# Performance work log

Hardware: AMD Instinct MI355X
Metric: run time of the kernel (lower is better)

Reference implementation:

```python
import jax, jax.numpy as jnp
from jax import lax
import numpy as np

OUTS = [5, 1, 2, 2, 1, 1, 1, 1]  # heatmap, conf, dxy, wh, dist, offset, severity, surface
OFFS = np.concatenate([[0], np.cumsum(OUTS)])
BN_EPS = 1e-5


def setup_inputs() -> dict:
    key = jax.random.key(0)
    ks = jax.random.split(key, 10)
    N, C, Hf, Wf = 16, 576, 12, 20
    f = jax.random.normal(ks[0], (N, C, Hf, Wf), jnp.float32)
    det_w1 = jax.random.normal(ks[1], (8, C, C, 3, 3), jnp.float32) * 0.02
    det_bn_g = 1.0 + 0.1 * jax.random.normal(ks[2], (8, C), jnp.float32)
    det_bn_b = 0.1 * jax.random.normal(ks[3], (8, C), jnp.float32)
    det_bn_m = 0.1 * jax.random.normal(ks[4], (8, C), jnp.float32)
    det_bn_v = jax.random.uniform(ks[5], (8, C), jnp.float32) + 0.5
    det_w2 = jax.random.normal(ks[6], (14, C), jnp.float32) * 0.05
    det_b2 = jax.random.normal(ks[7], (14,), jnp.float32) * 0.05
    lin_W = jax.random.normal(ks[8], (10, C), jnp.float32) * 0.05
    lin_b = jnp.zeros((10,), jnp.float32)
    return dict(f=f, det_w1=det_w1, det_bn_g=det_bn_g, det_bn_b=det_bn_b,
                det_bn_m=det_bn_m, det_bn_v=det_bn_v, det_w2=det_w2, det_b2=det_b2,
                lin_W=lin_W, lin_b=lin_b, frame_w=640, frame_h=384)


def _head(f, w1, g, b, m, v, w2, b2):
    # conv3x3 (no bias) -> BN (inference) -> SiLU -> conv1x1
    dn = ('NCHW', 'OIHW', 'NCHW')
    h = lax.conv_general_dilated(f, w1, (1, 1), 'SAME', dimension_numbers=dn)
    scale = g * lax.rsqrt(v + BN_EPS)
    h = h * scale[None, :, None, None] + (b - m * scale)[None, :, None, None]
    h = h * jax.nn.sigmoid(h)  # SiLU
    return jnp.einsum('nchw,oc->nohw', h, w2) + b2[None, :, None, None]


def _forward(f, det_w1, det_bn_g, det_bn_b, det_bn_m, det_bn_v, det_w2, det_b2,
             lin_W, lin_b, frame_w, frame_h, max_dets=20):
    N, C, Hf, Wf = f.shape
    eps = 1e-5
    # ---- legacy single-hazard head from pooled features ----
    f1 = f.mean(axis=(2, 3))                      # [N, 576]  (AdaptiveAvgPool2d(1))
    lin = f1 @ lin_W.T + lin_b                    # [N, 10]
    conf = jnp.clip(jax.nn.sigmoid(lin[:, 0:1]), eps, 1.0 - eps)
    type_log = lin[:, 1:6]
    dist_m = jax.nn.sigmoid(lin[:, 6:7]) * 3.0
    offset = jnp.tanh(lin[:, 7:8])
    severity = jnp.clip(jax.nn.sigmoid(lin[:, 8:9]), eps, 1.0 - eps)
    surface = jnp.clip(jax.nn.sigmoid(lin[:, 9:10]), eps, 1.0 - eps)
    type_id = jnp.argmax(type_log, axis=1, keepdims=True).astype(f.dtype)
    single_out = jnp.concatenate([conf, type_id, dist_m, offset, severity, surface], axis=1)

    # ---- dense per-pixel heads ----
    maps = []
    for i in range(8):
        o0, o1 = int(OFFS[i]), int(OFFS[i + 1])
        maps.append(_head(f, det_w1[i], det_bn_g[i], det_bn_b[i],
                          det_bn_m[i], det_bn_v[i], det_w2[o0:o1], det_b2[o0:o1]))
    heat = jax.nn.sigmoid(maps[0])                # [N,5,H,W]
    conf_d = jax.nn.sigmoid(maps[1])              # [N,1,H,W]
    dxy = jax.nn.sigmoid(maps[2])                 # [N,2,H,W]
    wh = jax.nn.sigmoid(maps[3])                  # [N,2,H,W]
    dist = jax.nn.sigmoid(maps[4]) * 3.0          # [N,1,H,W]
    offsm = jnp.tanh(maps[5])
    sev = jax.nn.sigmoid(maps[6])
    surf = jax.nn.sigmoid(maps[7])

    # ---- per-class topk decode ----
    score_flat = (conf_d * heat).reshape(N, 5, Hf * Wf)
    k = min(max_dets, Hf * Wf)
    topk_scores, topk_idx = lax.top_k(score_flat, k)          # [N,5,k]
    top_scores = topk_scores.reshape(N, -1)                    # [N,5k]
    top_class = jnp.broadcast_to(jnp.arange(5, dtype=f.dtype)[None, :, None], (N, 5, k)).reshape(N, -1)
    idx_flat = topk_idx.reshape(N, -1)                          # [N,5k]
    y_idx = (idx_flat // Wf).astype(f.dtype)
    x_idx = (idx_flat % Wf).astype(f.dtype)

    g1 = lambda m: jnp.take_along_axis(m.reshape(N, -1), idx_flat, axis=1)
    gx, gy = g1(dxy[:, 0]), g1(dxy[:, 1])
    gw, gh = g1(wh[:, 0]), g1(wh[:, 1])
    gdist, goffs = g1(dist), g1(offsm)
    gsev, gsurf = g1(sev), g1(surf)

    stride_x = frame_w / Wf
    stride_y = frame_h / Hf
    cx = jnp.clip(x_idx + gx, 0, Wf - 1) * stride_x
    cy = jnp.clip(y_idx + gy, 0, Hf - 1) * stride_y
    bw = jnp.clip(gw, 0, 1) * frame_w
    bh = jnp.clip(gh, 0, 1) * frame_h
    x1 = jnp.clip(cx - bw / 2, 0, frame_w - 1)
    y1 = jnp.clip(cy - bh / 2, 0, frame_h - 1)
    x2 = jnp.clip(cx + bw / 2, 0, frame_w - 1)
    y2 = jnp.clip(cy + bh / 2, 0, frame_h - 1)

    dets = jnp.stack([top_scores, top_class, gdist, goffs, gsev, gsurf, x1, y1, x2, y2], axis=-1)  # [N,5k,10]
    order = jnp.argsort(dets[:, :, 2], axis=-1)   # ascending distance (nearest first)
    dets_sorted = jnp.take_along_axis(dets, order[:, :, None], axis=1)
    dets_out = dets_sorted[:, :max_dets, :]        # [N,K,10]
    return single_out, dets_out


def reference(f, det_w1, det_bn_g, det_bn_b, det_bn_m, det_bn_v, det_w2, det_b2,
              lin_W, lin_b, frame_w, frame_h):
    return _forward(f, det_w1, det_bn_g, det_bn_b, det_bn_m, det_bn_v,
                    det_w2, det_b2, lin_W, lin_b, frame_w, frame_h)
```

## Files before the change

### kernel.cpp

```cpp
#include <hip/hip_runtime.h>
#include <math.h>

#define NB 16
#define CC 576
#define HH 12
#define WW 20
#define PP 240
#define MM 3840
#define NHEAD 8
#define HALO 22

typedef __attribute__((ext_vector_type(8))) short short8;
typedef __attribute__((ext_vector_type(4))) float floatx4;
typedef unsigned short ushort_t;

__device__ __forceinline__ float sigmoidf_(float x) {
    return 1.0f / (1.0f + expf(-x));
}
__device__ __forceinline__ unsigned short f2bf(float x) {
    union { float f; unsigned u; } v; v.f = x;
    unsigned r = v.u + 0x7fff + ((v.u >> 16) & 1);
    return (unsigned short)(r >> 16);
}
__device__ __forceinline__ float bf2f(unsigned short b) {
    union { float f; unsigned u; } v; v.u = ((unsigned)b) << 16;
    return v.f;
}

__global__ __launch_bounds__(256) void k_single(const float* __restrict__ f1sum,
                                                const float* __restrict__ linW,
                                                const float* __restrict__ linb,
                                                float* __restrict__ out) {
    int n = blockIdx.x;
    __shared__ float lin[10];
    int t = threadIdx.x;
    int lane = t & 63, wave = t >> 6;
    const float inv = 1.0f / PP;
    for (int o = wave; o < 10; o += 4) {
        const float* wrow = linW + o * CC;
        float s = 0.f;
        for (int c = lane; c < CC; c += 64)
            s = fmaf(f1sum[n * CC + c] * inv, wrow[c], s);
        #pragma unroll
        for (int off = 32; off; off >>= 1) s += __shfl_xor(s, off, 64);
        if (lane == 0) lin[o] = s + linb[o];
    }
    __syncthreads();
    if (t == 0) {
        const float eps = 1e-5f;
        float conf = sigmoidf_(lin[0]);
        conf = fminf(fmaxf(conf, eps), 1.f - eps);
        int best = 0; float bv = lin[1];
        #pragma unroll
        for (int j = 1; j < 5; ++j) { if (lin[1 + j] > bv) { bv = lin[1 + j]; best = j; } }
        float dist = 3.f * sigmoidf_(lin[6]);
        float offs = tanhf(lin[7]);
        float sev  = fminf(fmaxf(sigmoidf_(lin[8]), eps), 1.f - eps);
        float surf = fminf(fmaxf(sigmoidf_(lin[9]), eps), 1.f - eps);
        float* o = out + n * 6;
        o[0] = conf; o[1] = (float)best; o[2] = dist;
        o[3] = offs; o[4] = sev; o[5] = surf;
    }
}

__global__ __launch_bounds__(256) void k_prep_f(const float* __restrict__ f,
                                                ushort_t* __restrict__ fhi,
                                                ushort_t* __restrict__ flo,
                                                float* __restrict__ f1sum) {
    __shared__ float tile[32][33];
    int c0 = blockIdx.x * 32, p0 = blockIdx.y * 32, n = blockIdx.z;
    int tp = threadIdx.x & 31, tc8 = threadIdx.x >> 5;
    for (int cc = tc8; cc < 32; cc += 8) {
        int p = p0 + tp;
        tile[cc][tp] = (p < PP) ? f[((size_t)n * CC + c0 + cc) * PP + p] : 0.f;
    }
    __syncthreads();
    if (threadIdx.x < 32) {
        float s = 0.f;
        #pragma unroll
        for (int pp = 0; pp < 32; ++pp) s += tile[threadIdx.x][pp];
        atomicAdd(&f1sum[n * CC + c0 + threadIdx.x], s);
    }
    int tcw = threadIdx.x & 31, tpw = threadIdx.x >> 5;
    for (int pp = tpw; pp < 32; pp += 8) {
        int p = p0 + pp;
        if (p < PP) {
            float v = tile[tcw][pp];
            unsigned short hi = f2bf(v);
            size_t o = ((size_t)n * PP + p) * CC + c0 + tcw;
            fhi[o] = hi;
            flo[o] = f2bf(v - bf2f(hi));
        }
    }
}

__global__ __launch_bounds__(256) void k_prep_w(const float* __restrict__ w1,
                                                ushort_t* __restrict__ whi,
                                                ushort_t* __restrict__ wlo) {
    __shared__ float ws[288 * 33];
    int b = blockIdx.x;
    int cib = b % 18;
    int rest = b / 18;
    int half = rest & 1;
    int hc = rest >> 1;
    int t = threadIdx.x;
    const float* src = w1
        + ((size_t)(hc / 9) * CC + (hc % 9) * 64 + half * 32) * (CC * 9)
        + (size_t)cib * 288;
    for (int i = t; i < 32 * 288; i += 256) {
        int co = i / 288, k = i - co * 288;
        ws[k * 33 + co] = src[(size_t)co * (CC * 9) + k];
    }
    __syncthreads();
    size_t obase = ((size_t)hc * 18 + cib) * 18432 + (size_t)half * 1024;
    for (int idx = t; idx < 9 * 2 * 64; idx += 256) {
        int tap = idx / 128, r = idx - tap * 128;
        int jj = r >> 6, lane = r & 63;
        int col = jj * 16 + (lane & 15);
        int krow = (lane >> 4) * 8;
        short8 vh, vl;
        #pragma unroll
        for (int e = 0; e < 8; ++e) {
            float v = ws[((krow + e) * 9 + tap) * 33 + col];
            unsigned short hi = f2bf(v);
            vh[e] = (short)hi;
            vl[e] = (short)f2bf(v - bf2f(hi));
        }
        size_t o = obase + (size_t)tap * 2048 + jj * 512 + lane * 8;
        *(short8*)(whi + o) = vh;
        *(short8*)(wlo + o) = vl;
    }
}

__global__ __launch_bounds__(256, 3) void k_conv_mfma(
        const ushort_t* __restrict__ fhi, const ushort_t* __restrict__ flo,
        const ushort_t* __restrict__ whi, const ushort_t* __restrict__ wlo,
        const float* __restrict__ w2,
        const float* __restrict__ bng, const float* __restrict__ bnb,
        const float* __restrict__ bnm, const float* __restrict__ bnv,
        float* __restrict__ maps) {
    __shared__ __align__(16) ushort_t Ah[1216 * 8];
    __shared__ __align__(16) ushort_t Al[1216 * 8];
    __shared__ ushort_t rowmap[9 * 256];

    int t = threadIdx.x;

    int bid = blockIdx.x;
    int xcd = bid & 7;
    int q = bid >> 3;
    int mt = q % 15;
    int slice = (q / 15) * 8 + xcd;
    int m0 = mt * 256;
    int c0b = slice % 9;
    int c0 = c0b * 64;
    int h  = slice / 9;

    int w = t >> 6, lane = t & 63;
    int quad = lane >> 4, l15 = lane & 15;
    int srow_lo = t & 15, sg = (t >> 4) & 3, srb = t >> 6;

    const ushort_t* bp_h = whi + (size_t)(h * 9 + c0b) * 331776 + lane * 8;
    const ushort_t* bp_l = wlo + (size_t)(h * 9 + c0b) * 331776 + lane * 8;

    short8 cbh[4], cbl[4];
    #pragma unroll
    for (int j = 0; j < 4; ++j) {
        cbh[j] = *(const short8*)(bp_h + j * 512);
        cbl[j] = *(const short8*)(bp_l + j * 512);
    }

    if (t < 32) {
        int arr = t >> 4, g = (t >> 2) & 3, rr = 12 + (t & 3);
        int idx = 18 * 64 + g * 16 + rr;
        short8 z = {0, 0, 0, 0, 0, 0, 0, 0};
        *(short8*)((arr ? Al : Ah) + idx * 8) = z;
    }
    for (int idx = t; idx < 9 * 256; idx += 256) {
        int tap = idx >> 8, ml = idx & 255;
        int m = m0 + ml;
        int p = m % PP;
        int y = p / WW, x = p - y * WW;
        int dy = tap / 3 - 1, dx = tap % 3 - 1;
        int yy = y + dy, xx = x + dx;
        int row;
        if ((unsigned)yy < (unsigned)HH && (unsigned)xx < (unsigned)WW)
            row = ml + dy * WW + dx + HALO;
        else
            row = 300 + (ml & 3);
        rowmap[idx] = (ushort_t)row;
    }
    __syncthreads();

    floatx4 acc[4][4];
    #pragma unroll
    for (int i = 0; i < 4; ++i)
        #pragma unroll
        for (int j = 0; j < 4; ++j) acc[i][j] = (floatx4){0.f, 0.f, 0.f, 0.f};

    for (int cib = 0; cib < 18; ++cib) {
        __syncthreads();
        int koff = cib * 32 + sg * 8;
        #pragma unroll
        for (int it = 0; it < 5; ++it) {
            int row = (srb + 4 * it) * 16 + srow_lo;
            if (row < 300) {
                int mg = m0 - HALO + row;
                int cidx = 256 * it + t;
                short8 vh = {0, 0, 0, 0, 0, 0, 0, 0};
                short8 vl = {0, 0, 0, 0, 0, 0, 0, 0};
                if ((unsigned)mg < (unsigned)MM) {
                    vh = *(const short8*)(fhi + (size_t)mg * CC + koff);
                    vl = *(const short8*)(flo + (size_t)mg * CC + koff);
                }
                *(short8*)(Ah + cidx * 8) = vh;
                *(short8*)(Al + cidx * 8) = vl;
            }
        }
        __syncthreads();
        for (int tap = 0; tap < 9; ++tap) {
            int step = cib * 9 + tap;
            short8 nbh[4], nbl[4];
            if (step < 161) {
                int nt = tap + 1, nc = cib;
                if (nt == 9) { nt = 0; ++nc; }
                size_t o = (size_t)nc * 18432 + (size_t)nt * 2048;
                #pragma unroll
                for (int j = 0; j < 4; ++j) {
                    nbh[j] = *(const short8*)(bp_h + o + j * 512);
                    nbl[j] = *(const short8*)(bp_l + o + j * 512);
                }
            }

            short8 ah[4], al[4];
            #pragma unroll
            for (int i = 0; i < 4; ++i) {
                int r = rowmap[tap * 256 + w * 64 + i * 16 + l15];
                int a16 = ((r >> 4) * 64 + quad * 16 + (r & 15)) * 8;
                ah[i] = *(const short8*)(Ah + a16);
                al[i] = *(const short8*)(Al + a16);
            }
            #pragma unroll
            for (int i = 0; i < 4; ++i)
                #pragma unroll
                for (int j = 0; j < 4; ++j) {
                    acc[i][j] = __builtin_amdgcn_mfma_f32_16x16x32_bf16(
                        ah[i], cbh[j], acc[i][j], 0, 0, 0);
                    acc[i][j] = __builtin_amdgcn_mfma_f32_16x16x32_bf16(
                        ah[i], cbl[j], acc[i][j], 0, 0, 0);
                    acc[i][j] = __builtin_amdgcn_mfma_f32_16x16x32_bf16(
                        al[i], cbh[j], acc[i][j], 0, 0, 0);
                }
            if (step < 161) {
                #pragma unroll
                for (int j = 0; j < 4; ++j) { cbh[j] = nbh[j]; cbl[j] = nbl[j]; }
            }
        }
    }

    float scale[4], shift[4];
    #pragma unroll
    for (int j = 0; j < 4; ++j) {
        int c = h * CC + c0 + j * 16 + l15;
        float g_ = bng[c], bb = bnb[c], bm = bnm[c], bv = bnv[c];
        scale[j] = g_ / sqrtf(bv + 1e-5f);
        shift[j] = bb - bm * scale[j];
    }
    #pragma unroll
    for (int i = 0; i < 4; ++i)
        #pragma unroll
        for (int j = 0; j < 4; ++j)
            #pragma unroll
            for (int r = 0; r < 4; ++r) {
                float hx = fmaf(acc[i][j][r], scale[j], shift[j]);
                acc[i][j][r] = hx * sigmoidf_(hx);
            }

    static const int OFFo[NHEAD + 1] = {0, 5, 6, 8, 10, 11, 12, 13, 14};
    int o0 = OFFo[h], o1 = OFFo[h + 1];
    for (int o = o0; o < o1; ++o) {
        float w2v[4];
        #pragma unroll
        for (int j = 0; j < 4; ++j) w2v[j] = w2[o * CC + c0 + j * 16 + l15];
        float pv[4][4];
        #pragma unroll
        for (int i = 0; i < 4; ++i)
            #pragma unroll
            for (int r = 0; r < 4; ++r) {
                float s = 0.f;
                #pragma unroll
                for (int j = 0; j < 4; ++j) s = fmaf(acc[i][j][r], w2v[j], s);
                pv[i][r] = s;
            }
        #pragma unroll
        for (int off = 1; off < 16; off <<= 1)
            #pragma unroll
            for (int i = 0; i < 4; ++i)
                #pragma unroll
                for (int r = 0; r < 4; ++r)
                    pv[i][r] += __shfl_xor(pv[i][r], off, 64);
        if (l15 == 0) {
            #pragma unroll
            for (int i = 0; i < 4; ++i)
                #pragma unroll
                for (int r = 0; r < 4; ++r) {
                    int m = m0 + w * 64 + i * 16 + quad * 4 + r;
                    int n = m / PP, p = m - n * PP;
                    atomicAdd(&maps[(n * 14 + o) * PP + p], pv[i][r]);
                }
        }
    }
}

__global__ __launch_bounds__(256) void k_decode(
        const float* __restrict__ maps,
        const float* __restrict__ b2,
        const int* __restrict__ fw_p, const int* __restrict__ fh_p,
        float* __restrict__ out) {
    int n = blockIdx.x;
    int t = threadIdx.x;
    __shared__ float ms[14][PP];
    __shared__ float sconf[PP];
    __shared__ float cscore[100];
    __shared__ int   cidx[100];
    __shared__ float dets[100][10];
    __shared__ float dvals[100];

    const float* mp = maps + (size_t)n * 14 * PP;
    for (int idx = t; idx < 14 * PP; idx += 256)
        ms[idx / PP][idx % PP] = mp[idx] + b2[idx / PP];
    __syncthreads();
    if (t < PP) sconf[t] = sigmoidf_(ms[5][t]);
    __syncthreads();

    int wv = t >> 6, lane = t & 63;
    for (int cls = wv; cls < 5; cls += 4) {
        float v[4]; int pi[4];
        #pragma unroll
        for (int j = 0; j < 4; ++j) {
            int p = lane + 64 * j;
            pi[j] = p;
            v[j] = (p < PP) ? sconf[p] * sigmoidf_(ms[cls][p]) : -1e30f;
        }
        for (int r = 0; r < 20; ++r) {
            float bv = v[0]; int bi = pi[0];
            #pragma unroll
            for (int j = 1; j < 4; ++j)
                if (v[j] > bv || (v[j] == bv && pi[j] < bi)) { bv = v[j]; bi = pi[j]; }
            float rv = bv; int ri = bi;
            #pragma unroll
            for (int off = 32; off; off >>= 1) {
                float ov = __shfl_xor(rv, off, 64);
                int   oi = __shfl_xor(ri, off, 64);
                if (ov > rv || (ov == rv && oi < ri)) { rv = ov; ri = oi; }
            }
            if (lane == 0) { cscore[cls * 20 + r] = rv; cidx[cls * 20 + r] = ri; }
            #pragma unroll
            for (int j = 0; j < 4; ++j) if (pi[j] == ri) v[j] = -1e30f;
        }
    }
    __syncthreads();

    if (t < 100) {
        int cls = t / 20;
        int p = cidx[t];
        int yi = p / WW, xi = p - yi * WW;
        float gx = sigmoidf_(ms[6][p]),  gy = sigmoidf_(ms[7][p]);
        float gw = sigmoidf_(ms[8][p]),  gh = sigmoidf_(ms[9][p]);
        float gd = 3.f * sigmoidf_(ms[10][p]);
        float go = tanhf(ms[11][p]);
        float gs = sigmoidf_(ms[12][p]);
        float gf = sigmoidf_(ms[13][p]);
        float fw = (float)fw_p[0], fh = (float)fh_p[0];
        float sx = fw / (float)WW, sy = fh / (float)HH;
        float cx = fminf(fmaxf((float)xi + gx, 0.f), (float)WW - 1.f) * sx;
        float cy = fminf(fmaxf((float)yi + gy, 0.f), (float)HH - 1.f) * sy;
        float bw = fminf(fmaxf(gw, 0.f), 1.f) * fw;
        float bh = fminf(fmaxf(gh, 0.f), 1.f) * fh;
        float x1 = fminf(fmaxf(cx - bw * 0.5f, 0.f), fw - 1.f);
        float y1 = fminf(fmaxf(cy - bh * 0.5f, 0.f), fh - 1.f);
        float x2 = fminf(fmaxf(cx + bw * 0.5f, 0.f), fw - 1.f);
        float y2 = fminf(fmaxf(cy + bh * 0.5f, 0.f), fh - 1.f);
        dets[t][0] = cscore[t]; dets[t][1] = (float)cls;
        dets[t][2] = gd; dets[t][3] = go; dets[t][4] = gs; dets[t][5] = gf;
        dets[t][6] = x1; dets[t][7] = y1; dets[t][8] = x2; dets[t][9] = y2;
        dvals[t] = gd;
    }
    __syncthreads();
    if (t < 100) {
        float d = dvals[t];
        int rank = 0;
        for (int l = 0; l < 100; ++l) {
            float dl = dvals[l];
            rank += (dl < d) || (dl == d && l < t);
        }
        if (rank < 20) {
            float* o = out + 96 + ((size_t)n * 20 + rank) * 10;
            #pragma unroll
            for (int q = 0; q < 10; ++q) o[q] = dets[t][q];
        }
    }
}

extern "C" void kernel_launch(void* const* d_in, const int* in_sizes, int n_in,
                              void* d_out, int out_size, void* d_ws, size_t ws_size,
                              hipStream_t stream) {
    const float* f    = (const float*)d_in[0];
    const float* w1   = (const float*)d_in[1];
    const float* bng  = (const float*)d_in[2];
    const float* bnb  = (const float*)d_in[3];
    const float* bnm  = (const float*)d_in[4];
    const float* bnv  = (const float*)d_in[5];
    const float* w2   = (const float*)d_in[6];
    const float* b2   = (const float*)d_in[7];
    const float* linW = (const float*)d_in[8];
    const float* linb = (const float*)d_in[9];
    const int*   fw   = (const int*)d_in[10];
    const int*   fh   = (const int*)d_in[11];
    float* out = (float*)d_out;

    const size_t w_elems = (size_t)NHEAD * 9 * CC * CC;
    const size_t f_elems = (size_t)MM * CC;

    ushort_t* ws_whi = (ushort_t*)d_ws;
    ushort_t* ws_wlo = ws_whi + w_elems;
    ushort_t* ws_fhi = ws_wlo + w_elems;
    ushort_t* ws_flo = ws_fhi + f_elems;
    float*    ws_maps = (float*)(ws_flo + f_elems);
    float*    ws_f1sum = (float*)d_ws;

    hipMemsetAsync(ws_f1sum, 0, (size_t)NB * CC * sizeof(float), stream);
    hipMemsetAsync(ws_maps, 0, (size_t)NB * 14 * PP * sizeof(float), stream);
    k_prep_f<<<dim3(CC / 32, (PP + 31) / 32, NB), 256, 0, stream>>>(
        f, ws_fhi, ws_flo, ws_f1sum);
    k_single<<<NB, 256, 0, stream>>>(ws_f1sum, linW, linb, out);
    k_prep_w<<<NHEAD * 9 * 2 * 18, 256, 0, stream>>>(w1, ws_whi, ws_wlo);
    k_conv_mfma<<<dim3(15 * 9 * NHEAD), 256, 0, stream>>>(
        ws_fhi, ws_flo, ws_whi, ws_wlo, w2, bng, bnb, bnm, bnv, ws_maps);
    k_decode<<<NB, 256, 0, stream>>>(ws_maps, b2, fw, fh, out);
}
```

Baseline: 730.6 us.

## Split conv block across 8 waves, halving per-wave output columns

```diff
diff --git a/kernel.cpp b/kernel.cpp
--- a/kernel.cpp
+++ b/kernel.cpp
@@ -132,7 +132,7 @@
     }
 }
 
-__global__ __launch_bounds__(256, 3) void k_conv_mfma(
+__global__ __launch_bounds__(512, 6) void k_conv_mfma(
         const ushort_t* __restrict__ fhi, const ushort_t* __restrict__ flo,
         const ushort_t* __restrict__ whi, const ushort_t* __restrict__ wlo,
         const float* __restrict__ w2,
@@ -155,18 +155,21 @@
     int c0 = c0b * 64;
     int h  = slice / 9;
 
-    int w = t >> 6, lane = t & 63;
+    int w8 = t >> 6, lane = t & 63;
+    int wq = w8 >> 1, wj = w8 & 1;
     int quad = lane >> 4, l15 = lane & 15;
-    int srow_lo = t & 15, sg = (t >> 4) & 3, srb = t >> 6;
-
-    const ushort_t* bp_h = whi + (size_t)(h * 9 + c0b) * 331776 + lane * 8;
-    const ushort_t* bp_l = wlo + (size_t)(h * 9 + c0b) * 331776 + lane * 8;
-
-    short8 cbh[4], cbl[4];
+    int srow_lo = t & 15, sg = (t >> 4) & 3, srb8 = t >> 6;
+
+    const ushort_t* bp_h = whi + (size_t)(h * 9 + c0b) * 331776
+                               + (size_t)(wj * 2) * 512 + lane * 8;
+    const ushort_t* bp_l = wlo + (size_t)(h * 9 + c0b) * 331776
+                               + (size_t)(wj * 2) * 512 + lane * 8;
+
+    short8 cbh[2], cbl[2];
     #pragma unroll
-    for (int j = 0; j < 4; ++j) {
-        cbh[j] = *(const short8*)(bp_h + j * 512);
-        cbl[j] = *(const short8*)(bp_l + j * 512);
+    for (int jj = 0; jj < 2; ++jj) {
+        cbh[jj] = *(const short8*)(bp_h + jj * 512);
+        cbl[jj] = *(const short8*)(bp_l + jj * 512);
     }
 
     if (t < 32) {
@@ -175,7 +178,7 @@
         short8 z = {0, 0, 0, 0, 0, 0, 0, 0};
         *(short8*)((arr ? Al : Ah) + idx * 8) = z;
     }
-    for (int idx = t; idx < 9 * 256; idx += 256) {
+    for (int idx = t; idx < 9 * 256; idx += 512) {
         int tap = idx >> 8, ml = idx & 255;
         int m = m0 + ml;
         int p = m % PP;
@@ -191,21 +194,21 @@
     }
     __syncthreads();
 
-    floatx4 acc[4][4];
+    floatx4 acc[4][2];
     #pragma unroll
     for (int i = 0; i < 4; ++i)
         #pragma unroll
-        for (int j = 0; j < 4; ++j) acc[i][j] = (floatx4){0.f, 0.f, 0.f, 0.f};
+        for (int jj = 0; jj < 2; ++jj) acc[i][jj] = (floatx4){0.f, 0.f, 0.f, 0.f};
 
     for (int cib = 0; cib < 18; ++cib) {
         __syncthreads();
         int koff = cib * 32 + sg * 8;
         #pragma unroll
-        for (int it = 0; it < 5; ++it) {
-            int row = (srb + 4 * it) * 16 + srow_lo;
+        for (int it = 0; it < 3; ++it) {
+            int row = (srb8 + 8 * it) * 16 + srow_lo;
             if (row < 300) {
                 int mg = m0 - HALO + row;
-                int cidx = 256 * it + t;
+                int cidx = 512 * it + t;
                 short8 vh = {0, 0, 0, 0, 0, 0, 0, 0};
                 short8 vl = {0, 0, 0, 0, 0, 0, 0, 0};
                 if ((unsigned)mg < (unsigned)MM) {
@@ -219,22 +222,22 @@
         __syncthreads();
         for (int tap = 0; tap < 9; ++tap) {
             int step = cib * 9 + tap;
-            short8 nbh[4], nbl[4];
+            short8 nbh[2], nbl[2];
             if (step < 161) {
                 int nt = tap + 1, nc = cib;
                 if (nt == 9) { nt = 0; ++nc; }
                 size_t o = (size_t)nc * 18432 + (size_t)nt * 2048;
                 #pragma unroll
-                for (int j = 0; j < 4; ++j) {
-                    nbh[j] = *(const short8*)(bp_h + o + j * 512);
-                    nbl[j] = *(const short8*)(bp_l + o + j * 512);
+                for (int jj = 0; jj < 2; ++jj) {
+                    nbh[jj] = *(const short8*)(bp_h + o + jj * 512);
+                    nbl[jj] = *(const short8*)(bp_l + o + jj * 512);
                 }
             }
 
             short8 ah[4], al[4];
             #pragma unroll
             for (int i = 0; i < 4; ++i) {
-                int r = rowmap[tap * 256 + w * 64 + i * 16 + l15];
+                int r = rowmap[tap * 256 + wq * 64 + i * 16 + l15];
                 int a16 = ((r >> 4) * 64 + quad * 16 + (r & 15)) * 8;
                 ah[i] = *(const short8*)(Ah + a16);
                 al[i] = *(const short8*)(Al + a16);
@@ -242,45 +245,46 @@
             #pragma unroll
             for (int i = 0; i < 4; ++i)
                 #pragma unroll
-                for (int j = 0; j < 4; ++j) {
-                    acc[i][j] = __builtin_amdgcn_mfma_f32_16x16x32_bf16(
-                        ah[i], cbh[j], acc[i][j], 0, 0, 0);
-                    acc[i][j] = __builtin_amdgcn_mfma_f32_16x16x32_bf16(
-                        ah[i], cbl[j], acc[i][j], 0, 0, 0);
-                    acc[i][j] = __builtin_amdgcn_mfma_f32_16x16x32_bf16(
-                        al[i], cbh[j], acc[i][j], 0, 0, 0);
+                for (int jj = 0; jj < 2; ++jj) {
+                    acc[i][jj] = __builtin_amdgcn_mfma_f32_16x16x32_bf16(
+                        ah[i], cbh[jj], acc[i][jj], 0, 0, 0);
+                    acc[i][jj] = __builtin_amdgcn_mfma_f32_16x16x32_bf16(
+                        ah[i], cbl[jj], acc[i][jj], 0, 0, 0);
+                    acc[i][jj] = __builtin_amdgcn_mfma_f32_16x16x32_bf16(
+                        al[i], cbh[jj], acc[i][jj], 0, 0, 0);
                 }
             if (step < 161) {
                 #pragma unroll
-                for (int j = 0; j < 4; ++j) { cbh[j] = nbh[j]; cbl[j] = nbl[j]; }
-            }
-        }
-    }
-
-    float scale[4], shift[4];
+                for (int jj = 0; jj < 2; ++jj) { cbh[jj] = nbh[jj]; cbl[jj] = nbl[jj]; }
+            }
+        }
+    }
+
+    float scale[2], shift[2];
     #pragma unroll
-    for (int j = 0; j < 4; ++j) {
-        int c = h * CC + c0 + j * 16 + l15;
+    for (int jj = 0; jj < 2; ++jj) {
+        int c = h * CC + c0 + (wj * 2 + jj) * 16 + l15;
         float g_ = bng[c], bb = bnb[c], bm = bnm[c], bv = bnv[c];
-        scale[j] = g_ / sqrtf(bv + 1e-5f);
-        shift[j] = bb - bm * scale[j];
+        scale[jj] = g_ / sqrtf(bv + 1e-5f);
+        shift[jj] = bb - bm * scale[jj];
     }
     #pragma unroll
     for (int i = 0; i < 4; ++i)
         #pragma unroll
-        for (int j = 0; j < 4; ++j)
+        for (int jj = 0; jj < 2; ++jj)
             #pragma unroll
             for (int r = 0; r < 4; ++r) {
-                float hx = fmaf(acc[i][j][r], scale[j], shift[j]);
-                acc[i][j][r] = hx * sigmoidf_(hx);
+                float hx = fmaf(acc[i][jj][r], scale[jj], shift[jj]);
+                acc[i][jj][r] = hx * sigmoidf_(hx);
             }
 
     static const int OFFo[NHEAD + 1] = {0, 5, 6, 8, 10, 11, 12, 13, 14};
     int o0 = OFFo[h], o1 = OFFo[h + 1];
     for (int o = o0; o < o1; ++o) {
-        float w2v[4];
-        #pragma unroll
-        for (int j = 0; j < 4; ++j) w2v[j] = w2[o * CC + c0 + j * 16 + l15];
+        float w2v[2];
+        #pragma unroll
+        for (int jj = 0; jj < 2; ++jj)
+            w2v[jj] = w2[o * CC + c0 + (wj * 2 + jj) * 16 + l15];
         float pv[4][4];
         #pragma unroll
         for (int i = 0; i < 4; ++i)
@@ -288,7 +292,8 @@
             for (int r = 0; r < 4; ++r) {
                 float s = 0.f;
                 #pragma unroll
-                for (int j = 0; j < 4; ++j) s = fmaf(acc[i][j][r], w2v[j], s);
+                for (int jj = 0; jj < 2; ++jj)
+                    s = fmaf(acc[i][jj][r], w2v[jj], s);
                 pv[i][r] = s;
             }
         #pragma unroll
@@ -303,7 +308,7 @@
             for (int i = 0; i < 4; ++i)
                 #pragma unroll
                 for (int r = 0; r < 4; ++r) {
-                    int m = m0 + w * 64 + i * 16 + quad * 4 + r;
+                    int m = m0 + wq * 64 + i * 16 + quad * 4 + r;
                     int n = m / PP, p = m - n * PP;
                     atomicAdd(&maps[(n * 14 + o) * PP + p], pv[i][r]);
                 }
@@ -434,7 +439,7 @@
         f, ws_fhi, ws_flo, ws_f1sum);
     k_single<<<NB, 256, 0, stream>>>(ws_f1sum, linW, linb, out);
     k_prep_w<<<NHEAD * 9 * 2 * 18, 256, 0, stream>>>(w1, ws_whi, ws_wlo);
-    k_conv_mfma<<<dim3(15 * 9 * NHEAD), 256, 0, stream>>>(
+    k_conv_mfma<<<dim3(15 * 9 * NHEAD), 512, 0, stream>>>(
         ws_fhi, ws_flo, ws_whi, ws_wlo, w2, bng, bnb, bnm, bnv, ws_maps);
     k_decode<<<NB, 256, 0, stream>>>(ws_maps, b2, fw, fh, out);
 }
```

Measured after the change: 866.0 us. +18.5%, slower.
